# Performance work log

Hardware: AMD Instinct MI355X
Metric: run time of the kernel (lower is better)

Reference implementation:

```python
import jax, jax.numpy as jnp
import numpy as np

B, V, J, NS, NE = 2048, 5023, 5, 300, 100
PARENTS = np.array([-1, 0, 1, 1, 1])  # FLAME kintree: neck<-global, jaw/eyes<-neck


def _rodrigues(rvecs):
    """Axis-angle [..., 3] -> rotation matrices [..., 3, 3] (smplx convention)."""
    angle = jnp.linalg.norm(rvecs + 1e-8, axis=-1, keepdims=True)  # [...,1]
    axis = rvecs / angle
    rx, ry, rz = axis[..., 0], axis[..., 1], axis[..., 2]
    z = jnp.zeros_like(rx)
    K = jnp.stack([z, -rz, ry, rz, z, -rx, -ry, rx, z], axis=-1)
    K = K.reshape(rvecs.shape[:-1] + (3, 3))
    s = jnp.sin(angle)[..., None]
    c = jnp.cos(angle)[..., None]
    eye = jnp.eye(3, dtype=rvecs.dtype)
    return eye + s * K + (1.0 - c) * jnp.matmul(K, K)


def setup_inputs() -> dict:
    key = jax.random.key(0)
    ks = jax.random.split(key, 12)
    jr = jax.random.uniform(ks[9], (J, V), dtype=jnp.float32)
    jr = jr / jnp.sum(jr, axis=1, keepdims=True)
    w = jax.random.uniform(ks[10], (V, J), dtype=jnp.float32)
    w = w / jnp.sum(w, axis=1, keepdims=True)  # skinning weights sum to 1
    return {
        'shape': 0.1 * jax.random.normal(ks[0], (B, NS), dtype=jnp.float32),
        'expr': 0.1 * jax.random.normal(ks[1], (B, NE), dtype=jnp.float32),
        'global_pose': 0.1 * jax.random.normal(ks[2], (B, 3), dtype=jnp.float32),
        'neck_pose': 0.1 * jax.random.normal(ks[3], (B, 3), dtype=jnp.float32),
        'jaw_pose': 0.1 * jax.random.normal(ks[4], (B, 3), dtype=jnp.float32),
        'eye_pose': 0.1 * jax.random.normal(ks[5], (B, 6), dtype=jnp.float32),
        'v_template': jax.random.normal(ks[6], (V, 3), dtype=jnp.float32),
        'shape_dirs': 0.01 * jax.random.normal(ks[7], (V, 3, NS + NE), dtype=jnp.float32),
        'pose_dirs': 0.01 * jax.random.normal(ks[8], (36, V * 3), dtype=jnp.float32),
        'J_regressor': jr,
        'lbs_weights': w,
        'parents': jnp.asarray(PARENTS, dtype=jnp.int32),
    }


def reference(shape, expr, global_pose, neck_pose, jaw_pose, eye_pose,
              v_template, shape_dirs, pose_dirs, J_regressor, lbs_weights, parents):
    b = shape.shape[0]
    betas = jnp.concatenate([shape, expr], axis=1)                       # [B, NS+NE]
    full_pose = jnp.concatenate([global_pose, neck_pose, jaw_pose, eye_pose], axis=1)  # [B, 15]

    # shape/expression blendshapes
    v_shaped = v_template[None] + jnp.einsum('bl,vkl->bvk', betas, shape_dirs)  # [B,V,3]
    joints = jnp.einsum('jv,bvk->bjk', J_regressor, v_shaped)                   # [B,J,3]

    # pose -> rotation matrices, pose blendshapes
    rot_mats = _rodrigues(full_pose.reshape(b, J, 3))                           # [B,J,3,3]
    eye3 = jnp.eye(3, dtype=rot_mats.dtype)
    pose_feature = (rot_mats[:, 1:] - eye3).reshape(b, (J - 1) * 9)             # [B,36]
    v_posed = v_shaped + (pose_feature @ pose_dirs).reshape(b, V, 3)

    # rigid transforms along kinematic tree (J=5, unrolled Python loop)
    par = PARENTS
    rel_joints = jnp.concatenate([joints[:, :1], joints[:, 1:] - joints[:, par[1:]]], axis=1)
    tm = jnp.concatenate([rot_mats, rel_joints[..., None]], axis=-1)            # [B,J,3,4]
    bottom = jnp.broadcast_to(jnp.array([0., 0., 0., 1.], tm.dtype), (b, J, 1, 4))
    tm4 = jnp.concatenate([tm, bottom], axis=-2)                                # [B,J,4,4]
    chain = [tm4[:, 0]]
    for i in range(1, J):
        chain.append(jnp.matmul(chain[int(par[i])], tm4[:, i]))
    transforms = jnp.stack(chain, axis=1)                                       # [B,J,4,4]

    joints_hom = jnp.concatenate([joints, jnp.zeros((b, J, 1), joints.dtype)], axis=-1)
    tj = jnp.einsum('bjxy,bjy->bjx', transforms, joints_hom)
    A = transforms.at[..., :, 3].add(-tj)  # relative transforms w.r.t. rest joints

    # linear blend skinning
    T = jnp.einsum('vj,bjxy->bvxy', lbs_weights, A)                             # [B,V,4,4]
    v_hom = jnp.concatenate([v_posed, jnp.ones((b, V, 1), v_posed.dtype)], axis=-1)
    verts = jnp.einsum('bvxy,bvy->bvx', T, v_hom)[..., :3]                      # [B,V,3]
    return verts, rot_mats
```

## Files before the change

kernel.cpp:

```cpp
#include <hip/hip_runtime.h>
#include <hip/hip_bf16.h>
#include <math.h>

#define B_    2048
#define V_    5023
#define N3    15069
#define VOFF  30861312

#define BM    256
#define BN    96
#define NKC   14
#define NBX   157
#define NBY   8

#define OFF_CBT    0
#define OFF_SDTT   458752
#define OFF_JSP    0
#define OFF_JS     3834880
#define OFF_JT     3840880
#define OFF_A      3840896

#define NCH 512
#define CHV 10

typedef __attribute__((ext_vector_type(8))) short short8;
typedef __attribute__((ext_vector_type(4))) float f32x4;

typedef __attribute__((address_space(1))) const void gvoid_t;
typedef __attribute__((address_space(3))) void lvoid_t;
#define GLDS16(g, l) __builtin_amdgcn_global_load_lds((gvoid_t*)(g), (lvoid_t*)(l), 16, 0, 0)

__global__ void __launch_bounds__(512) k_js(
    const float* __restrict__ Jreg, const float* __restrict__ SD,
    const float* __restrict__ VT, float* __restrict__ ws) {
    int ch = blockIdx.x;
    int v0 = ch * CHV;
    int t = threadIdx.x;
    __shared__ float jw[5][CHV];
    for (int s = t; s < 5 * CHV; s += 512) {
        int j = s / CHV, vi = s % CHV;
        int v = v0 + vi;
        jw[j][vi] = (v < V_) ? Jreg[j * V_ + v] : 0.f;
    }
    __syncthreads();
    int nv = min(V_ - v0, CHV);
    if (t < 400) {
        float acc[15];
        #pragma unroll
        for (int i = 0; i < 15; ++i) acc[i] = 0.f;
        for (int vi = 0; vi < nv; ++vi) {
            int v = v0 + vi;
            float s0 = SD[(v * 3 + 0) * 400 + t];
            float s1 = SD[(v * 3 + 1) * 400 + t];
            float s2 = SD[(v * 3 + 2) * 400 + t];
            #pragma unroll
            for (int j = 0; j < 5; ++j) {
                float jr = jw[j][vi];
                acc[j * 3 + 0] += jr * s0;
                acc[j * 3 + 1] += jr * s1;
                acc[j * 3 + 2] += jr * s2;
            }
        }
        #pragma unroll
        for (int i = 0; i < 15; ++i)
            ws[OFF_JSP + ch * 6016 + i * 400 + t] = acc[i];
    } else if (t >= 448 && t < 463) {
        int jk = t - 448, j = jk / 3, k = jk % 3;
        float a = 0.f;
        for (int vi = 0; vi < nv; ++vi)
            a += jw[j][vi] * VT[(v0 + vi) * 3 + k];
        ws[OFF_JSP + ch * 6016 + 6000 + jk] = a;
    }
}

__global__ void k_js_reduce(float* __restrict__ ws) {
    int r = blockIdx.x * 256 + threadIdx.x;
    if (r >= 6016) return;
    float s = 0.f;
    for (int ch = 0; ch < NCH; ++ch) s += ws[OFF_JSP + ch * 6016 + r];
    if (r < 6000) ws[OFF_JS + r] = s;
    else if (r < 6015) ws[OFF_JT + (r - 6000)] = s;
}

__global__ void __launch_bounds__(256) k_sdt_lds(
    const float* __restrict__ SD, const float* __restrict__ PD,
    float* __restrict__ ws) {
    __shared__ __hip_bfloat16 lb[16][456];
    int bid = blockIdx.x;
    int bx = bid / 6, jl = bid % 6;
    int n0 = bx * 96 + jl * 16;
    int tid = threadIdx.x;
    for (int s = tid; s < 16 * 400; s += 256) {
        int r = s / 400, c = s % 400;
        int n = n0 + r;
        lb[r][c] = __float2bfloat16((n < N3) ? SD[n * 400 + c] : 0.f);
    }
    for (int s = tid; s < 36 * 16; s += 256) {
        int p = s / 16, r = s % 16;
        int n = n0 + r;
        lb[r][400 + p] = __float2bfloat16((n < N3) ? PD[p * N3 + n] : 0.f);
    }
    for (int s = tid; s < 12 * 16; s += 256) {
        int c = s / 16, r = s % 16;
        lb[r][436 + c] = __float2bfloat16(0.f);
    }
    __syncthreads();
    uint4* sdtt = (uint4*)((char*)ws + (size_t)OFF_SDTT * 4);
    for (int s = tid; s < NKC * 64; s += 256) {
        int kc = s >> 6, lane = s & 63;
        int r = lane & 15;
        int k0 = kc * 32 + (lane >> 4) * 8;
        uint4 val = *(const uint4*)&lb[r][k0];
        sdtt[((size_t)(bx * NKC + kc) * 6 + jl) * 64 + lane] = val;
    }
}

__global__ void k_cbt_tiled(const float* __restrict__ sh, const float* __restrict__ ex,
                            float* __restrict__ ws) {
    int id = blockIdx.x * 256 + threadIdx.x;
    if (id >= NBY * NKC * 16 * 64) return;
    int lane = id & 63;
    int t = id >> 6;
    int mf = t & 15; t >>= 4;
    int kc = t % NKC, by = t / NKC;
    int b = by * BM + mf * 16 + (lane & 15);
    int k0 = kc * 32 + (lane >> 4) * 8;
    union { __hip_bfloat16 h[8]; uint4 u; } pk;
    #pragma unroll
    for (int e = 0; e < 8; ++e) {
        int k = k0 + e;
        float v = 0.f;
        if (k < 300) v = sh[b * 300 + k];
        else if (k < 400) v = ex[b * 100 + (k - 300)];
        pk.h[e] = __float2bfloat16(v);
    }
    ((uint4*)ws)[id] = pk.u;
}

__device__ __forceinline__ int cbt_idx(int b, int k) {
    int by = b >> 8, mf = (b & 255) >> 4, cr = b & 15;
    int kc = k >> 5, kg = (k & 31) >> 3, e = k & 7;
    return (((by * NKC + kc) * 16 + mf) * 64 + kg * 16 + cr) * 8 + e;
}

__device__ __forceinline__ void rodrigues(float rx, float ry, float rz, float* R) {
    float ax = rx + 1e-8f, ay = ry + 1e-8f, az = rz + 1e-8f;
    float ang = sqrtf(ax * ax + ay * ay + az * az);
    float inv = 1.f / ang;
    float ux = rx * inv, uy = ry * inv, uz = rz * inv;
    float s = sinf(ang), c = cosf(ang), m = 1.f - c;
    R[0] = 1.f + m * (-uz * uz - uy * uy);
    R[1] = -s * uz + m * ux * uy;
    R[2] =  s * uy + m * ux * uz;
    R[3] =  s * uz + m * ux * uy;
    R[4] = 1.f + m * (-uz * uz - ux * ux);
    R[5] = -s * ux + m * uy * uz;
    R[6] = -s * uy + m * ux * uz;
    R[7] =  s * ux + m * uy * uz;
    R[8] = 1.f + m * (-uy * uy - ux * ux);
}

__global__ void __launch_bounds__(256) k_batch(
    const float* __restrict__ gp, const float* __restrict__ npo,
    const float* __restrict__ jp, const float* __restrict__ ep,
    const float* __restrict__ sh, const float* __restrict__ ex,
    float* __restrict__ out, float* __restrict__ ws) {
    __shared__ float js_l[6000];
    __shared__ float jtp[4][64][15];
    int tid = threadIdx.x;
    int w = tid >> 6, lane = tid & 63;
    int b = blockIdx.x * 64 + lane;
    for (int s = tid; s < 6000; s += 256) js_l[s] = ws[OFF_JS + s];
    __syncthreads();
    float p15[15];
    #pragma unroll
    for (int q = 0; q < 15; ++q) p15[q] = 0.f;
    for (int i = 0; i < 100; ++i) {
        int k = 100 * w + i;
        float cl = (w < 3) ? sh[b * 300 + k] : ex[b * 100 + i];
        #pragma unroll
        for (int q = 0; q < 15; ++q) p15[q] += js_l[q * 400 + k] * cl;
    }
    #pragma unroll
    for (int q = 0; q < 15; ++q) jtp[w][lane][q] = p15[q];
    __syncthreads();
    if (w != 0) return;

    float jt[15];
    #pragma unroll
    for (int q = 0; q < 15; ++q)
        jt[q] = ws[OFF_JT + q] + jtp[0][lane][q] + jtp[1][lane][q]
              + jtp[2][lane][q] + jtp[3][lane][q];

    float R[5][9];
    rodrigues(gp[b * 3], gp[b * 3 + 1], gp[b * 3 + 2], R[0]);
    rodrigues(npo[b * 3], npo[b * 3 + 1], npo[b * 3 + 2], R[1]);
    rodrigues(jp[b * 3], jp[b * 3 + 1], jp[b * 3 + 2], R[2]);
    rodrigues(ep[b * 6], ep[b * 6 + 1], ep[b * 6 + 2], R[3]);
    rodrigues(ep[b * 6 + 3], ep[b * 6 + 4], ep[b * 6 + 5], R[4]);
    for (int j = 0; j < 5; ++j)
        for (int i = 0; i < 9; ++i)
            out[VOFF + b * 45 + j * 9 + i] = R[j][i];
    __hip_bfloat16* cb = (__hip_bfloat16*)ws;
    for (int j = 1; j < 5; ++j)
        for (int i = 0; i < 9; ++i)
            cb[cbt_idx(b, 400 + (j - 1) * 9 + i)] =
                __float2bfloat16(R[j][i] - ((i == 0 || i == 4 || i == 8) ? 1.f : 0.f));

    const int par[5] = {0, 0, 1, 1, 1};
    float rel[5][3];
    for (int k = 0; k < 3; ++k) rel[0][k] = jt[k];
    for (int j = 1; j < 5; ++j)
        for (int k = 0; k < 3; ++k) rel[j][k] = jt[j * 3 + k] - jt[par[j] * 3 + k];
    float Rc[5][9], tc[5][3];
    for (int i = 0; i < 9; ++i) Rc[0][i] = R[0][i];
    for (int k = 0; k < 3; ++k) tc[0][k] = rel[0][k];
    for (int j = 1; j < 5; ++j) {
        int p = par[j];
        for (int r = 0; r < 3; ++r) {
            for (int c2 = 0; c2 < 3; ++c2) {
                float s = 0.f;
                for (int m = 0; m < 3; ++m) s += Rc[p][r * 3 + m] * R[j][m * 3 + c2];
                Rc[j][r * 3 + c2] = s;
            }
            float tv = 0.f;
            for (int m = 0; m < 3; ++m) tv += Rc[p][r * 3 + m] * rel[j][m];
            tc[j][r] = tv + tc[p][r];
        }
    }
    for (int j = 0; j < 5; ++j)
        for (int r = 0; r < 3; ++r) {
            float tj = 0.f;
            for (int m = 0; m < 3; ++m) tj += Rc[j][r * 3 + m] * jt[j * 3 + m];
            ws[OFF_A + b * 60 + j * 12 + r * 4 + 0] = Rc[j][r * 3 + 0];
            ws[OFF_A + b * 60 + j * 12 + r * 4 + 1] = Rc[j][r * 3 + 1];
            ws[OFF_A + b * 60 + j * 12 + r * 4 + 2] = Rc[j][r * 3 + 2];
            ws[OFF_A + b * 60 + j * 12 + r * 4 + 3] = tc[j][r] - tj;
        }
}

__global__ void __launch_bounds__(256, 3) k_gemm_lbs(
    const float* __restrict__ VT, const float* __restrict__ W,
    const float* __restrict__ ws, float* __restrict__ out) {
    __shared__ __align__(16) char smem[45056];

    const char* cbt  = (const char*)ws;
    const char* sdtt = (const char*)ws + (size_t)OFF_SDTT * 4;
    const float* Amat = ws + OFF_A;

    int flat = blockIdx.x;
    int nid = (flat & 7) * 157 + (flat >> 3);
    int bx = nid >> 3, by = nid & 7;
    int n0 = bx * BN, b0 = by * BM, v0 = bx * 32;

    int tid = threadIdx.x;
    int w = tid >> 6, lane = tid & 63;

    const char* Aglb = cbt + (size_t)(by * NKC) * 16384;
    const char* Bglb = sdtt + (size_t)(bx * NKC) * 6144;

    auto stage = [&](int kc, int p) {
        char* lA = smem + p * 22528;
        char* lB = lA + 16384;
        const char* ga = Aglb + (size_t)kc * 16384;
        const char* gb = Bglb + (size_t)kc * 6144;
        #pragma unroll
        for (int c = 0; c < 4; ++c) {
            int ch = 4 * w + c;
            GLDS16(ga + ch * 1024 + lane * 16, lA + ch * 1024);
        }
        if (w < 3) {
            #pragma unroll
            for (int c = 0; c < 2; ++c) {
                int ch = 2 * w + c;
                GLDS16(gb + ch * 1024 + lane * 16, lB + ch * 1024);
            }
        }
    };

    stage(0, 0);
    stage(1, 1);

    f32x4 acc[4][6];
    #pragma unroll
    for (int m = 0; m < 4; ++m)
        #pragma unroll
        for (int j = 0; j < 6; ++j) acc[m][j] = (f32x4){0.f, 0.f, 0.f, 0.f};

    for (int kc = 0; kc < NKC; ++kc) {
        int p = kc & 1;
        if (kc < NKC - 1) {
            if (w < 3) asm volatile("s_waitcnt vmcnt(6)" ::: "memory");
            else       asm volatile("s_waitcnt vmcnt(4)" ::: "memory");
        } else {
            asm volatile("s_waitcnt vmcnt(0)" ::: "memory");
        }
        __builtin_amdgcn_s_barrier();
        const char* lA = smem + p * 22528;
        const char* lB = lA + 16384;
        short8 af[4];
        #pragma unroll
        for (int m = 0; m < 4; ++m)
            af[m] = *(const short8*)(lA + (4 * w + m) * 1024 + lane * 16);
        #pragma unroll
        for (int j = 0; j < 6; ++j) {
            short8 bf = *(const short8*)(lB + j * 1024 + lane * 16);
            #pragma unroll
            for (int m = 0; m < 4; ++m)
                acc[m][j] = __builtin_amdgcn_mfma_f32_16x16x32_bf16(af[m], bf, acc[m][j], 0, 0, 0);
        }
        __builtin_amdgcn_s_barrier();
        if (kc + 2 < NKC) stage(kc + 2, p);
    }

    float vt6[6];
    #pragma unroll
    for (int j = 0; j < 6; ++j) {
        int n = n0 + 16 * j + (lane & 15);
        vt6[j] = (n < N3) ? VT[n] : 0.f;
    }
    int vl = tid & 31, v = v0 + vl;
    bool vok = v < V_;
    float w5[5] = {0.f, 0.f, 0.f, 0.f, 0.f};
    if (vok)
        #pragma unroll
        for (int j = 0; j < 5; ++j) w5[j] = W[v * 5 + j];

    float* Am = (float*)smem;
    float* Ps = (float*)(smem + 15872);

    #pragma unroll
    for (int h = 0; h < 4; ++h) {
        const float4* Ag = (const float4*)&Amat[(b0 + 64 * h) * 60];
        for (int s = tid; s < 960; s += 256)
            ((float4*)Am)[s] = Ag[s];
        if (w == h) {
            #pragma unroll
            for (int j = 0; j < 6; ++j) {
                int col = 16 * j + (lane & 15);
                #pragma unroll
                for (int m = 0; m < 4; ++m) {
                    int lrow = 16 * m + 4 * (lane >> 4);
                    #pragma unroll
                    for (int i = 0; i < 4; ++i)
                        Ps[(lrow + i) * 98 + col] = acc[m][j][i] + vt6[j];
                }
            }
        }
        __syncthreads();
        #pragma unroll 2
        for (int q = 0; q < 8; ++q) {
            int bl = (tid >> 5) + 8 * q;
            float px = Ps[bl * 98 + 3 * vl + 0];
            float py = Ps[bl * 98 + 3 * vl + 1];
            float pz = Ps[bl * 98 + 3 * vl + 2];
            if (vok) {
                const float4* Aq = (const float4*)&Am[bl * 60];
                float4 t0 = {0,0,0,0}, t1 = {0,0,0,0}, t2 = {0,0,0,0};
                #pragma unroll
                for (int j = 0; j < 5; ++j) {
                    float wj = w5[j];
                    float4 a0 = Aq[j * 3 + 0], a1 = Aq[j * 3 + 1], a2 = Aq[j * 3 + 2];
                    t0.x += wj * a0.x; t0.y += wj * a0.y; t0.z += wj * a0.z; t0.w += wj * a0.w;
                    t1.x += wj * a1.x; t1.y += wj * a1.y; t1.z += wj * a1.z; t1.w += wj * a1.w;
                    t2.x += wj * a2.x; t2.y += wj * a2.y; t2.z += wj * a2.z; t2.w += wj * a2.w;
                }
                int b = b0 + 64 * h + bl;
                int ob = b * N3 + v * 3;
                out[ob + 0] = t0.x * px + t0.y * py + t0.z * pz + t0.w;
                out[ob + 1] = t1.x * px + t1.y * py + t1.z * pz + t1.w;
                out[ob + 2] = t2.x * px + t2.y * py + t2.z * pz + t2.w;
            }
        }
        __syncthreads();
    }
}

extern "C" void kernel_launch(void* const* d_in, const int* in_sizes, int n_in,
                              void* d_out, int out_size, void* d_ws, size_t ws_size,
                              hipStream_t stream) {
    const float* shape = (const float*)d_in[0];
    const float* expr  = (const float*)d_in[1];
    const float* gpose = (const float*)d_in[2];
    const float* npose = (const float*)d_in[3];
    const float* jpose = (const float*)d_in[4];
    const float* epose = (const float*)d_in[5];
    const float* vt    = (const float*)d_in[6];
    const float* sd    = (const float*)d_in[7];
    const float* pd    = (const float*)d_in[8];
    const float* jreg  = (const float*)d_in[9];
    const float* w     = (const float*)d_in[10];
    float* out = (float*)d_out;
    float* ws  = (float*)d_ws;

    k_js<<<NCH, 512, 0, stream>>>(jreg, sd, vt, ws);
    k_js_reduce<<<24, 256, 0, stream>>>(ws);
    k_sdt_lds<<<NBX * 6, 256, 0, stream>>>(sd, pd, ws);
    k_cbt_tiled<<<(NBY * NKC * 16 * 64 + 255) / 256, 256, 0, stream>>>(shape, expr, ws);
    k_batch<<<32, 256, 0, stream>>>(gpose, npose, jpose, epose, shape, expr, out, ws);
    k_gemm_lbs<<<NBX * NBY, 256, 0, stream>>>(vt, w, ws, out);
}
```

Measured before the change: 124.5 us.

## Fuse joint-shape regression into shape-dir bf16 repack kernel to share loads

```diff
diff --git a/kernel.cpp b/kernel.cpp
--- a/kernel.cpp
+++ b/kernel.cpp
@@ -15,13 +15,10 @@
 
 #define OFF_CBT    0
 #define OFF_SDTT   458752
-#define OFF_JSP    0
 #define OFF_JS     3834880
 #define OFF_JT     3840880
 #define OFF_A      3840896
-
-#define NCH 512
-#define CHV 10
+#define OFF_JSP    4000000
 
 typedef __attribute__((ext_vector_type(8))) short short8;
 typedef __attribute__((ext_vector_type(4))) float f32x4;
@@ -30,29 +27,54 @@
 typedef __attribute__((address_space(3))) void lvoid_t;
 #define GLDS16(g, l) __builtin_amdgcn_global_load_lds((gvoid_t*)(g), (lvoid_t*)(l), 16, 0, 0)
 
-__global__ void __launch_bounds__(512) k_js(
-    const float* __restrict__ Jreg, const float* __restrict__ SD,
-    const float* __restrict__ VT, float* __restrict__ ws) {
-    int ch = blockIdx.x;
-    int v0 = ch * CHV;
-    int t = threadIdx.x;
-    __shared__ float jw[5][CHV];
-    for (int s = t; s < 5 * CHV; s += 512) {
-        int j = s / CHV, vi = s % CHV;
+__global__ void __launch_bounds__(512) k_sdt_js(
+    const float* __restrict__ SD, const float* __restrict__ PD,
+    const float* __restrict__ Jreg, const float* __restrict__ VT,
+    float* __restrict__ ws) {
+    __shared__ __hip_bfloat16 lb[96][456];
+    __shared__ float jw[5][32];
+    int bx = blockIdx.x;
+    int n0 = bx * 96;
+    int v0 = bx * 32;
+    int tid = threadIdx.x;
+    for (int s = tid; s < 5 * 32; s += 512) {
+        int j = s >> 5, vi = s & 31;
         int v = v0 + vi;
         jw[j][vi] = (v < V_) ? Jreg[j * V_ + v] : 0.f;
     }
+    for (int s = tid; s < 96 * 400; s += 512) {
+        int r = s / 400, c = s % 400;
+        int n = n0 + r;
+        lb[r][c] = __float2bfloat16((n < N3) ? SD[n * 400 + c] : 0.f);
+    }
+    for (int s = tid; s < 36 * 96; s += 512) {
+        int p = s / 96, r = s % 96;
+        int n = n0 + r;
+        lb[r][400 + p] = __float2bfloat16((n < N3) ? PD[p * N3 + n] : 0.f);
+    }
+    for (int s = tid; s < 12 * 96; s += 512) {
+        int c = s / 96, r = s % 96;
+        lb[r][436 + c] = __float2bfloat16(0.f);
+    }
     __syncthreads();
-    int nv = min(V_ - v0, CHV);
-    if (t < 400) {
+    uint4* sdtt = (uint4*)((char*)ws + (size_t)OFF_SDTT * 4);
+    for (int s = tid; s < NKC * 6 * 64; s += 512) {
+        int lane = s & 63;
+        int g = s >> 6;
+        int jl = g % 6, kc = g / 6;
+        int r = jl * 16 + (lane & 15);
+        int k0 = kc * 32 + (lane >> 4) * 8;
+        uint4 val = *(const uint4*)&lb[r][k0];
+        sdtt[((size_t)(bx * NKC + kc) * 6 + jl) * 64 + lane] = val;
+    }
+    if (tid < 400) {
         float acc[15];
         #pragma unroll
         for (int i = 0; i < 15; ++i) acc[i] = 0.f;
-        for (int vi = 0; vi < nv; ++vi) {
-            int v = v0 + vi;
-            float s0 = SD[(v * 3 + 0) * 400 + t];
-            float s1 = SD[(v * 3 + 1) * 400 + t];
-            float s2 = SD[(v * 3 + 2) * 400 + t];
+        for (int vi = 0; vi < 32; ++vi) {
+            float s0 = __bfloat162float(lb[vi * 3 + 0][tid]);
+            float s1 = __bfloat162float(lb[vi * 3 + 1][tid]);
+            float s2 = __bfloat162float(lb[vi * 3 + 2][tid]);
             #pragma unroll
             for (int j = 0; j < 5; ++j) {
                 float jr = jw[j][vi];
@@ -63,13 +85,15 @@
         }
         #pragma unroll
         for (int i = 0; i < 15; ++i)
-            ws[OFF_JSP + ch * 6016 + i * 400 + t] = acc[i];
-    } else if (t >= 448 && t < 463) {
-        int jk = t - 448, j = jk / 3, k = jk % 3;
+            ws[OFF_JSP + bx * 6016 + i * 400 + tid] = acc[i];
+    } else if (tid >= 448 && tid < 463) {
+        int jk = tid - 448, j = jk / 3, k = jk % 3;
         float a = 0.f;
-        for (int vi = 0; vi < nv; ++vi)
-            a += jw[j][vi] * VT[(v0 + vi) * 3 + k];
-        ws[OFF_JSP + ch * 6016 + 6000 + jk] = a;
+        for (int vi = 0; vi < 32; ++vi) {
+            int v = v0 + vi;
+            if (v < V_) a += jw[j][vi] * VT[v * 3 + k];
+        }
+        ws[OFF_JSP + bx * 6016 + 6000 + jk] = a;
     }
 }
 
@@ -77,42 +101,9 @@
     int r = blockIdx.x * 256 + threadIdx.x;
     if (r >= 6016) return;
     float s = 0.f;
-    for (int ch = 0; ch < NCH; ++ch) s += ws[OFF_JSP + ch * 6016 + r];
+    for (int ch = 0; ch < NBX; ++ch) s += ws[OFF_JSP + ch * 6016 + r];
     if (r < 6000) ws[OFF_JS + r] = s;
     else if (r < 6015) ws[OFF_JT + (r - 6000)] = s;
-}
-
-__global__ void __launch_bounds__(256) k_sdt_lds(
-    const float* __restrict__ SD, const float* __restrict__ PD,
-    float* __restrict__ ws) {
-    __shared__ __hip_bfloat16 lb[16][456];
-    int bid = blockIdx.x;
-    int bx = bid / 6, jl = bid % 6;
-    int n0 = bx * 96 + jl * 16;
-    int tid = threadIdx.x;
-    for (int s = tid; s < 16 * 400; s += 256) {
-        int r = s / 400, c = s % 400;
-        int n = n0 + r;
-        lb[r][c] = __float2bfloat16((n < N3) ? SD[n * 400 + c] : 0.f);
-    }
-    for (int s = tid; s < 36 * 16; s += 256) {
-        int p = s / 16, r = s % 16;
-        int n = n0 + r;
-        lb[r][400 + p] = __float2bfloat16((n < N3) ? PD[p * N3 + n] : 0.f);
-    }
-    for (int s = tid; s < 12 * 16; s += 256) {
-        int c = s / 16, r = s % 16;
-        lb[r][436 + c] = __float2bfloat16(0.f);
-    }
-    __syncthreads();
-    uint4* sdtt = (uint4*)((char*)ws + (size_t)OFF_SDTT * 4);
-    for (int s = tid; s < NKC * 64; s += 256) {
-        int kc = s >> 6, lane = s & 63;
-        int r = lane & 15;
-        int k0 = kc * 32 + (lane >> 4) * 8;
-        uint4 val = *(const uint4*)&lb[r][k0];
-        sdtt[((size_t)(bx * NKC + kc) * 6 + jl) * 64 + lane] = val;
-    }
 }
 
 __global__ void k_cbt_tiled(const float* __restrict__ sh, const float* __restrict__ ex,
@@ -393,9 +384,8 @@
     float* out = (float*)d_out;
     float* ws  = (float*)d_ws;
 
-    k_js<<<NCH, 512, 0, stream>>>(jreg, sd, vt, ws);
+    k_sdt_js<<<NBX, 512, 0, stream>>>(sd, pd, jreg, vt, ws);
     k_js_reduce<<<24, 256, 0, stream>>>(ws);
-    k_sdt_lds<<<NBX * 6, 256, 0, stream>>>(sd, pd, ws);
     k_cbt_tiled<<<(NBY * NKC * 16 * 64 + 255) / 256, 256, 0, stream>>>(shape, expr, ws);
     k_batch<<<32, 256, 0, stream>>>(gpose, npose, jpose, epose, shape, expr, out, ws);
     k_gemm_lbs<<<NBX * NBY, 256, 0, stream>>>(vt, w, ws, out);
```

New measurement: 135.8 us. 1.09x slower.
